# Kernel tuning notes

Hardware: AMD Instinct MI355X
Metric: run time of the kernel (lower is better)

The kernel has to match this reference:

```python
import jax, jax.numpy as jnp
import numpy as np

B, T = 2, 2048
V, C, H = 32000, 1024, 16
HS = C // H  # 64
W_SCALE = 0.02


def setup_inputs() -> dict:
    key = jax.random.key(0)
    ks = jax.random.split(key, 8)
    x = jax.random.randint(ks[0], (B, T), 0, V)
    tok_emb = jax.random.normal(ks[1], (V, C), jnp.float32) * W_SCALE
    pos_emb = jax.random.normal(ks[2], (T, C), jnp.float32) * W_SCALE
    wq = jax.random.normal(ks[3], (H, C, HS), jnp.float32) * W_SCALE
    wk = jax.random.normal(ks[4], (H, C, HS), jnp.float32) * W_SCALE
    wv = jax.random.normal(ks[5], (H, C, HS), jnp.float32) * W_SCALE
    bq = jnp.zeros((H, HS), jnp.float32)
    bk = jnp.zeros((H, HS), jnp.float32)
    bv = jnp.zeros((H, HS), jnp.float32)
    w_head = jax.random.normal(ks[6], (C, V), jnp.float32) * W_SCALE
    b_head = jnp.zeros((V,), jnp.float32)
    return dict(x=x, tok_emb=tok_emb, pos_emb=pos_emb, wq=wq, bq=bq,
                wk=wk, bk=bk, wv=wv, bv=bv, w_head=w_head, b_head=b_head)


def reference(x, tok_emb, pos_emb, wq, bq, wk, bk, wv, bv, w_head, b_head):
    Bx, Tx = x.shape
    Cx = tok_emb.shape[1]
    h = tok_emb[x] + pos_emb[:Tx]  # [B,T,C]
    # all heads batched: per-head Linear layers stacked on leading H axis
    q = jnp.einsum('btc,hcd->bhtd', h, wq) + bq[None, :, None, :]
    k = jnp.einsum('btc,hcd->bhtd', h, wk) + bk[None, :, None, :]
    v = jnp.einsum('btc,hcd->bhtd', h, wv) + bv[None, :, None, :]
    # NOTE: original scales by n_embd**-0.5 (full C), not head_size**-0.5
    att = jnp.einsum('bhtd,bhsd->bhts', q, k) * (Cx ** -0.5)
    causal = jnp.tril(jnp.ones((Tx, Tx), dtype=bool))
    att = jnp.where(causal, att, jnp.finfo(att.dtype).min)
    att = jax.nn.softmax(att, axis=-1)
    y = jnp.einsum('bhts,bhsd->bhtd', att, v)  # [B,H,T,HS]
    y = jnp.transpose(y, (0, 2, 1, 3)).reshape(Bx, Tx, Cx)  # concat heads
    logits = jnp.einsum('btc,cv->btv', y, w_head) + b_head  # [B,T,V]
    return logits
```

## Files before the change

kernel.cpp:

```cpp
#include <hip/hip_runtime.h>

#define T_SEQ 2048
#define C_DIM 1024
#define H_N   16
#define HS_D  64
#define V_DIM 32000

typedef float f32x4 __attribute__((ext_vector_type(4)));
typedef __bf16 bf16x8 __attribute__((ext_vector_type(8)));
typedef unsigned short us4 __attribute__((ext_vector_type(4)));
typedef unsigned short us8 __attribute__((ext_vector_type(8)));

__device__ inline unsigned short f2bf(float f) {
  unsigned int u = __float_as_uint(f);
  u = (u + 0x7FFFu + ((u >> 16) & 1u)) >> 16;
  return (unsigned short)u;
}

__global__ __launch_bounds__(256) void embed_kernel(
    const int* __restrict__ x, const float* __restrict__ tok,
    const float* __restrict__ pos, unsigned short* __restrict__ h) {
  int idx = blockIdx.x * 256 + threadIdx.x;
  int bt = idx >> 8;
  int c4 = (idx & 255) * 4;
  int t = bt & (T_SEQ - 1);
  int tokid = x[bt];
  f32x4 a = *(const f32x4*)(tok + (size_t)tokid * C_DIM + c4);
  f32x4 b = *(const f32x4*)(pos + (size_t)t * C_DIM + c4);
  f32x4 s = a + b;
  us4 o;
  o[0] = f2bf(s[0]); o[1] = f2bf(s[1]); o[2] = f2bf(s[2]); o[3] = f2bf(s[3]);
  *(us4*)(h + (size_t)bt * C_DIM + c4) = o;
}

__global__ __launch_bounds__(256) void repack_qkv(
    const float* __restrict__ wq, const float* __restrict__ wk, const float* __restrict__ wv,
    const float* __restrict__ bq, const float* __restrict__ bk, const float* __restrict__ bv,
    unsigned short* __restrict__ wt, float* __restrict__ biasp) {
  int which = blockIdx.y;
  const float* w = (which == 0) ? wq : (which == 1) ? wk : wv;
  int i = blockIdx.x * 256 + threadIdx.x;
  int d = i & 63;
  int c = (i >> 6) & (C_DIM - 1);
  int hh = i >> 16;
  int n = which * 1024 + hh * 64 + d;
  wt[(size_t)n * C_DIM + c] = f2bf(w[i]);
  if (c == 0) {
    const float* bb = (which == 0) ? bq : (which == 1) ? bk : bv;
    biasp[n] = bb[hh * 64 + d];
  }
}

__global__ __launch_bounds__(256) void repack_whead(
    const float* __restrict__ wh, unsigned short* __restrict__ wht) {
  __shared__ float tile[64][65];
  int v0 = blockIdx.x * 64;
  int c0 = blockIdx.y * 64;
  int tr = threadIdx.x >> 6;
  int tc = threadIdx.x & 63;
#pragma unroll
  for (int i = 0; i < 16; ++i) {
    int r = i * 4 + tr;
    tile[r][tc] = wh[(size_t)(c0 + r) * V_DIM + v0 + tc];
  }
  __syncthreads();
#pragma unroll
  for (int i = 0; i < 16; ++i) {
    int vr = i * 4 + tr;
    wht[(size_t)(v0 + vr) * C_DIM + c0 + tc] = f2bf(tile[tc][vr]);
  }
}

__global__ __launch_bounds__(256) void gemm_bf16(
    const unsigned short* __restrict__ A, const unsigned short* __restrict__ Bt,
    const float* __restrict__ bias, float* __restrict__ Cout, int N) {
  const int K = 1024;
  __shared__ unsigned short As[128 * 32];
  __shared__ unsigned short Bs[128 * 32];
  int tid = threadIdx.x;
  int lane = tid & 63, wvi = tid >> 6;
  int m0 = blockIdx.y * 128, n0 = blockIdx.x * 128;
  int wmm = (wvi >> 1) * 64, wnn = (wvi & 1) * 64;
  int r16 = lane & 15, gg = lane >> 4;
  f32x4 acc[4][4] = {};

  for (int k0 = 0; k0 < K; k0 += 32) {
#pragma unroll
    for (int it = 0; it < 2; ++it) {
      int ch = it * 256 + wvi * 64 + lane;
      int row = ch >> 2, cc = (ch & 3) * 8;
      const unsigned short* ga = A + (size_t)(m0 + row) * K + k0 + cc;
      __builtin_amdgcn_global_load_lds(
          (const __attribute__((address_space(1))) void*)ga,
          (__attribute__((address_space(3))) void*)&As[ch * 8], 16, 0, 0);
      const unsigned short* gb = Bt + (size_t)(n0 + row) * K + k0 + cc;
      __builtin_amdgcn_global_load_lds(
          (const __attribute__((address_space(1))) void*)gb,
          (__attribute__((address_space(3))) void*)&Bs[ch * 8], 16, 0, 0);
    }
    __syncthreads();
    bf16x8 fa[4], fb[4];
#pragma unroll
    for (int m = 0; m < 4; ++m)
      fa[m] = *(const bf16x8*)&As[(wmm + m * 16 + r16) * 32 + gg * 8];
#pragma unroll
    for (int n = 0; n < 4; ++n)
      fb[n] = *(const bf16x8*)&Bs[(wnn + n * 16 + r16) * 32 + gg * 8];
#pragma unroll
    for (int m = 0; m < 4; ++m)
#pragma unroll
      for (int n = 0; n < 4; ++n)
        acc[m][n] = __builtin_amdgcn_mfma_f32_16x16x32_bf16(fa[m], fb[n], acc[m][n], 0, 0, 0);
    __syncthreads();
  }
#pragma unroll
  for (int m = 0; m < 4; ++m) {
    int row = m0 + wmm + m * 16 + gg * 4;
#pragma unroll
    for (int n = 0; n < 4; ++n) {
      int col = n0 + wnn + n * 16 + r16;
      float bval = bias[col];
#pragma unroll
      for (int j = 0; j < 4; ++j)
        Cout[(size_t)(row + j) * N + col] = acc[m][n][j] + bval;
    }
  }
}

#define GK 1024
#define GNT 16

__global__ __launch_bounds__(512, 1) void gemm256(
    const unsigned short* __restrict__ A, const unsigned short* __restrict__ Bt,
    const float* __restrict__ bias, float* __restrict__ Cout, int N, int Mtiles) {
  __shared__ unsigned short As[2][256 * 64];
  __shared__ unsigned short Bs[2][256 * 64];
  int tid = threadIdx.x;
  int lane = tid & 63;
  int wid = tid >> 6;
  int wm = wid >> 2, wn = wid & 3;
  int l16 = lane & 15, g = lane >> 4;
  int swz = l16 & 7;

  int cpx = gridDim.x >> 3;
  int lin = blockIdx.x;
  int wg = (lin & 7) * cpx + (lin >> 3);
  int m0 = (wg % Mtiles) * 256;
  int n0 = (wg / Mtiles) * 256;

  auto stageA2 = [&](int kt, int mh) {
    unsigned short* lds = As[kt & 1];
#pragma unroll
    for (int q = 0; q < 2; ++q) {
      int chunk = q * 512 + tid;
      int rr = chunk >> 3;
      int row = (rr & 63) + ((rr >> 6) << 7) + mh * 64;
      int cpos = chunk & 7;
      int c = cpos ^ (row & 7);
      const unsigned short* src = A + (size_t)(m0 + row) * GK + kt * 64 + c * 8;
      __builtin_amdgcn_global_load_lds(
          (const __attribute__((address_space(1))) void*)src,
          (__attribute__((address_space(3))) void*)(lds + row * 64 + cpos * 8), 16, 0, 0);
    }
  };
  auto stageB4 = [&](int kt) {
    unsigned short* lds = Bs[kt & 1];
#pragma unroll
    for (int q = 0; q < 4; ++q) {
      int chunk = q * 512 + tid;
      int row = chunk >> 3;
      int cpos = chunk & 7;
      int c = cpos ^ (row & 7);
      const unsigned short* src = Bt + (size_t)(n0 + row) * GK + kt * 64 + c * 8;
      __builtin_amdgcn_global_load_lds(
          (const __attribute__((address_space(1))) void*)src,
          (__attribute__((address_space(3))) void*)(lds + row * 64 + cpos * 8), 16, 0, 0);
    }
  };

  stageA2(0, 0); stageB4(0);
  stageA2(0, 1);
  stageA2(1, 0); stageB4(1);
  asm volatile("s_waitcnt vmcnt(8)" ::: "memory");
  asm volatile("s_barrier" ::: "memory");

  f32x4 acc[8][4] = {};

  for (int t = 0; t < GNT; ++t) {
    const char* Ab = (const char*)As[t & 1];
    const char* Bb = (const char*)Bs[t & 1];
    bf16x8 bA[4][2], bB[4][2];

#pragma unroll
    for (int mi = 0; mi < 4; ++mi) {
      int row = wm * 128 + mi * 16 + l16;
#pragma unroll
      for (int kk = 0; kk < 2; ++kk)
        bA[mi][kk] = *(const bf16x8*)(Ab + row * 128 + (((kk * 4 + g) ^ swz) * 16));
    }
#pragma unroll
    for (int ni = 0; ni < 4; ++ni) {
      int row = wn * 64 + ni * 16 + l16;
#pragma unroll
      for (int kk = 0; kk < 2; ++kk)
        bB[ni][kk] = *(const bf16x8*)(Bb + row * 128 + (((kk * 4 + g) ^ swz) * 16));
    }
    if (t + 1 < GNT) stageA2(t + 1, 1);
    asm volatile("s_barrier" ::: "memory");
    asm volatile("s_waitcnt lgkmcnt(0)" ::: "memory");
    __builtin_amdgcn_sched_barrier(0);
    __builtin_amdgcn_s_setprio(1);
#pragma unroll
    for (int mi = 0; mi < 4; ++mi)
#pragma unroll
      for (int ni = 0; ni < 4; ++ni)
#pragma unroll
        for (int kk = 0; kk < 2; ++kk)
          acc[mi][ni] = __builtin_amdgcn_mfma_f32_16x16x32_bf16(bA[mi][kk], bB[ni][kk], acc[mi][ni], 0, 0, 0);
    __builtin_amdgcn_s_setprio(0);
    if (t + 1 < GNT) asm volatile("s_waitcnt vmcnt(8)" ::: "memory");
    else             asm volatile("s_waitcnt vmcnt(0)" ::: "memory");
    asm volatile("s_barrier" ::: "memory");

#pragma unroll
    for (int mi = 0; mi < 4; ++mi) {
      int row = wm * 128 + 64 + mi * 16 + l16;
#pragma unroll
      for (int kk = 0; kk < 2; ++kk)
        bA[mi][kk] = *(const bf16x8*)(Ab + row * 128 + (((kk * 4 + g) ^ swz) * 16));
    }
    if (t + 2 < GNT) { stageA2(t + 2, 0); stageB4(t + 2); }
    asm volatile("s_barrier" ::: "memory");
    asm volatile("s_waitcnt lgkmcnt(0)" ::: "memory");
    __builtin_amdgcn_sched_barrier(0);
    __builtin_amdgcn_s_setprio(1);
#pragma unroll
    for (int mi = 0; mi < 4; ++mi)
#pragma unroll
      for (int ni = 0; ni < 4; ++ni)
#pragma unroll
        for (int kk = 0; kk < 2; ++kk)
          acc[4 + mi][ni] = __builtin_amdgcn_mfma_f32_16x16x32_bf16(bA[mi][kk], bB[ni][kk], acc[4 + mi][ni], 0, 0, 0);
    __builtin_amdgcn_s_setprio(0);
    if (t + 2 < GNT)      asm volatile("s_waitcnt vmcnt(8)" ::: "memory");
    else if (t + 2 == GNT) asm volatile("s_waitcnt vmcnt(2)" ::: "memory");
    asm volatile("s_barrier" ::: "memory");
  }

#pragma unroll
  for (int mf = 0; mf < 8; ++mf) {
    int row = m0 + wm * 128 + mf * 16 + g * 4;
#pragma unroll
    for (int n = 0; n < 4; ++n) {
      int col = n0 + wn * 64 + n * 16 + l16;
      float bv = bias[col];
#pragma unroll
      for (int j = 0; j < 4; ++j)
        Cout[(size_t)(row + j) * N + col] = acc[mf][n][j] + bv;
    }
  }
}

__global__ __launch_bounds__(256) void attn_mfma(
    const float* __restrict__ qkv, unsigned short* __restrict__ y) {
  __shared__ char lds[24576];
  char* Kl = lds;
  char* Vl = lds + 8192;
  char* Pl = lds + 16384;

  int bh = blockIdx.y;
  int b = bh >> 4, h = bh & 15;
  int qb = (T_SEQ / 64 - 1) - blockIdx.x;
  int tid = threadIdx.x;
  int lane = tid & 63, w = tid >> 6;
  int l16 = lane & 15, g = lane >> 4;
  size_t bT = (size_t)b * T_SEQ;
  const float scale = 0.03125f;

  bf16x8 qf[2];
  {
    const float* qrow = qkv + (bT + qb * 64 + w * 16 + l16) * 3072 + h * 64;
#pragma unroll
    for (int kk = 0; kk < 2; ++kk) {
      f32x4 a = *(const f32x4*)(qrow + kk * 32 + g * 8);
      f32x4 c = *(const f32x4*)(qrow + kk * 32 + g * 8 + 4);
      us8 o;
      o[0] = f2bf(a[0]); o[1] = f2bf(a[1]); o[2] = f2bf(a[2]); o[3] = f2bf(a[3]);
      o[4] = f2bf(c[0]); o[5] = f2bf(c[1]); o[6] = f2bf(c[2]); o[7] = f2bf(c[3]);
      qf[kk] = *(bf16x8*)&o;
    }
  }

  f32x4 yacc[4] = {};
  float mrun[4], lrun[4];
#pragma unroll
  for (int j = 0; j < 4; ++j) { mrun[j] = -3.0e38f; lrun[j] = 0.f; }

  int srow = tid >> 2;
  int c0 = (tid & 3) * 16;

  for (int kb = 0; kb <= qb; ++kb) {
    {
      const float* kp = qkv + (bT + kb * 64 + srow) * 3072 + 1024 + h * 64 + c0;
      f32x4 k0 = *(const f32x4*)(kp + 0);
      f32x4 k1 = *(const f32x4*)(kp + 4);
      f32x4 k2 = *(const f32x4*)(kp + 8);
      f32x4 k3 = *(const f32x4*)(kp + 12);
      us8 pa, pb;
      pa[0]=f2bf(k0[0]); pa[1]=f2bf(k0[1]); pa[2]=f2bf(k0[2]); pa[3]=f2bf(k0[3]);
      pa[4]=f2bf(k1[0]); pa[5]=f2bf(k1[1]); pa[6]=f2bf(k1[2]); pa[7]=f2bf(k1[3]);
      pb[0]=f2bf(k2[0]); pb[1]=f2bf(k2[1]); pb[2]=f2bf(k2[2]); pb[3]=f2bf(k2[3]);
      pb[4]=f2bf(k3[0]); pb[5]=f2bf(k3[1]); pb[6]=f2bf(k3[2]); pb[7]=f2bf(k3[3]);
      *(us8*)(Kl + ((srow * 128 + c0 * 2)      ^ ((srow & 7) << 4))) = pa;
      *(us8*)(Kl + ((srow * 128 + c0 * 2 + 16) ^ ((srow & 7) << 4))) = pb;
      const float* vp = kp + 1024;
      f32x4 v0 = *(const f32x4*)(vp + 0);
      f32x4 v1 = *(const f32x4*)(vp + 4);
      f32x4 v2 = *(const f32x4*)(vp + 8);
      f32x4 v3 = *(const f32x4*)(vp + 12);
      float vals[16] = {v0[0],v0[1],v0[2],v0[3], v1[0],v1[1],v1[2],v1[3],
                        v2[0],v2[1],v2[2],v2[3], v3[0],v3[1],v3[2],v3[3]};
#pragma unroll
      for (int i = 0; i < 16; ++i) {
        int ch = c0 + i;
        *(unsigned short*)(Vl + ((ch * 128 + srow * 2) ^ ((ch & 7) << 4))) = f2bf(vals[i]);
      }
    }
    __syncthreads();

    f32x4 s[4] = {};
#pragma unroll
    for (int kk = 0; kk < 2; ++kk)
#pragma unroll
      for (int n = 0; n < 4; ++n) {
        int krow = n * 16 + l16;
        bf16x8 fb = *(const bf16x8*)(Kl + ((krow * 128 + (kk * 32 + g * 8) * 2) ^ ((krow & 7) << 4)));
        s[n] = __builtin_amdgcn_mfma_f32_16x16x32_bf16(qf[kk], fb, s[n], 0, 0, 0);
      }

    bool diag = (kb == qb);
    float pr[4][4];
    float corr[4];
#pragma unroll
    for (int j = 0; j < 4; ++j) {
      int rloc = w * 16 + g * 4 + j;
      float m = -3.0e38f;
#pragma unroll
      for (int n = 0; n < 4; ++n) {
        float v = s[n][j] * scale;
        if (diag && (n * 16 + l16) > rloc) v = -3.0e38f;
        pr[n][j] = v;
        m = fmaxf(m, v);
      }
      m = fmaxf(m, __shfl_xor(m, 1));
      m = fmaxf(m, __shfl_xor(m, 2));
      m = fmaxf(m, __shfl_xor(m, 4));
      m = fmaxf(m, __shfl_xor(m, 8));
      float mn = fmaxf(mrun[j], m);
      corr[j] = __expf(mrun[j] - mn);
      mrun[j] = mn;
      float ps = 0.f;
#pragma unroll
      for (int n = 0; n < 4; ++n) {
        float e = __expf(pr[n][j] - mn);
        pr[n][j] = e;
        ps += e;
      }
      ps += __shfl_xor(ps, 1);
      ps += __shfl_xor(ps, 2);
      ps += __shfl_xor(ps, 4);
      ps += __shfl_xor(ps, 8);
      lrun[j] = lrun[j] * corr[j] + ps;
    }
#pragma unroll
    for (int n = 0; n < 4; ++n)
#pragma unroll
      for (int j = 0; j < 4; ++j)
        yacc[n][j] *= corr[j];

#pragma unroll
    for (int j = 0; j < 4; ++j) {
      int row = w * 16 + g * 4 + j;
#pragma unroll
      for (int n = 0; n < 4; ++n)
        *(unsigned short*)(Pl + ((row * 128 + (n * 16 + l16) * 2) ^ ((row & 7) << 4))) = f2bf(pr[n][j]);
    }

#pragma unroll
    for (int kk = 0; kk < 2; ++kk) {
      int prow = w * 16 + l16;
      bf16x8 fa = *(const bf16x8*)(Pl + ((prow * 128 + (kk * 32 + g * 8) * 2) ^ ((prow & 7) << 4)));
#pragma unroll
      for (int n = 0; n < 4; ++n) {
        int vrow = n * 16 + l16;
        bf16x8 fb = *(const bf16x8*)(Vl + ((vrow * 128 + (kk * 32 + g * 8) * 2) ^ ((vrow & 7) << 4)));
        yacc[n] = __builtin_amdgcn_mfma_f32_16x16x32_bf16(fa, fb, yacc[n], 0, 0, 0);
      }
    }
    __syncthreads();
  }

#pragma unroll
  for (int j = 0; j < 4; ++j) {
    float inv = 1.0f / lrun[j];
    int row = qb * 64 + w * 16 + g * 4 + j;
    unsigned short* yo = y + (bT + row) * C_DIM + h * 64;
#pragma unroll
    for (int n = 0; n < 4; ++n)
      yo[n * 16 + l16] = f2bf(yacc[n][j] * inv);
  }
}

extern "C" void kernel_launch(void* const* d_in, const int* in_sizes, int n_in,
                              void* d_out, int out_size, void* d_ws, size_t ws_size,
                              hipStream_t stream) {
  const int*   x    = (const int*)d_in[0];
  const float* tok  = (const float*)d_in[1];
  const float* pos  = (const float*)d_in[2];
  const float* wq   = (const float*)d_in[3];
  const float* bq   = (const float*)d_in[4];
  const float* wk   = (const float*)d_in[5];
  const float* bk   = (const float*)d_in[6];
  const float* wv   = (const float*)d_in[7];
  const float* bv   = (const float*)d_in[8];
  const float* wh   = (const float*)d_in[9];
  const float* bhd  = (const float*)d_in[10];
  float* out = (float*)d_out;

  char* ws = (char*)d_ws;
  size_t off = 0;
  auto alloc = [&](size_t bytes) {
    void* p = ws + off;
    off += (bytes + 255) & ~(size_t)255;
    return p;
  };
  unsigned short* h_bf    = (unsigned short*)alloc((size_t)4096 * 1024 * 2);
  unsigned short* wqkv_t  = (unsigned short*)alloc((size_t)3072 * 1024 * 2);
  float*          qbias   = (float*)alloc((size_t)3072 * 4);
  unsigned short* wh_t    = (unsigned short*)alloc((size_t)V_DIM * 1024 * 2);
  float*          qkv     = (float*)alloc((size_t)4096 * 3072 * 4);
  unsigned short* ybf     = (unsigned short*)alloc((size_t)4096 * 1024 * 2);

  embed_kernel<<<4096, 256, 0, stream>>>(x, tok, pos, h_bf);
  repack_qkv<<<dim3(4096, 3), 256, 0, stream>>>(wq, wk, wv, bq, bk, bv, wqkv_t, qbias);
  repack_whead<<<dim3(V_DIM / 64, 16), 256, 0, stream>>>(wh, wh_t);
  gemm_bf16<<<dim3(3072 / 128, 4096 / 128), 256, 0, stream>>>(h_bf, wqkv_t, qbias, qkv, 3072);
  attn_mfma<<<dim3(T_SEQ / 64, 2 * H_N), 256, 0, stream>>>(qkv, ybf);
  gemm256<<<2000, 512, 0, stream>>>(ybf, wh_t, bhd, out, V_DIM, 16);
}
```

Measured before the change: 649.6 us.

## Emit bf16 QKV, pre-transpose V, and double-buffer K/V loads in attention

The QKV GEMM now writes bf16 instead of fp32, which halves its output traffic and removes the per-iteration fp32-to-bf16 conversion in attention. A new kernel transposes V per head into a contiguous layout so that attention can stage K and V directly into LDS with asynchronous global-to-LDS loads. Those loads are double-buffered, prefetching the next block while the current one is computed, and explicit waitcnt/barrier handle synchronisation. The cost is an extra kernel launch, an extra V buffer in memory, and more LDS per block.

```diff
diff --git a/kernel.cpp b/kernel.cpp
--- a/kernel.cpp
+++ b/kernel.cpp
@@ -71,9 +71,9 @@
   }
 }
 
-__global__ __launch_bounds__(256) void gemm_bf16(
+__global__ __launch_bounds__(256) void gemm_bf16_o16(
     const unsigned short* __restrict__ A, const unsigned short* __restrict__ Bt,
-    const float* __restrict__ bias, float* __restrict__ Cout, int N) {
+    const float* __restrict__ bias, unsigned short* __restrict__ Cout, int N) {
   const int K = 1024;
   __shared__ unsigned short As[128 * 32];
   __shared__ unsigned short Bs[128 * 32];
@@ -122,9 +122,29 @@
       float bval = bias[col];
 #pragma unroll
       for (int j = 0; j < 4; ++j)
-        Cout[(size_t)(row + j) * N + col] = acc[m][n][j] + bval;
-    }
-  }
+        Cout[(size_t)(row + j) * N + col] = f2bf(acc[m][n][j] + bval);
+    }
+  }
+}
+
+__global__ __launch_bounds__(256) void transpose_v(
+    const unsigned short* __restrict__ qkv, unsigned short* __restrict__ vt) {
+  __shared__ unsigned short tile[64][72];
+  int bh = blockIdx.y;
+  int b = bh >> 4, h = bh & 15;
+  int tb = blockIdx.x;
+  int r = threadIdx.x >> 2;
+  int c0 = (threadIdx.x & 3) * 16;
+  const unsigned short* src = qkv + ((size_t)(b * T_SEQ) + tb * 64 + r) * 3072 + 2048 + h * 64 + c0;
+  *(us8*)&tile[r][c0] = *(const us8*)src;
+  *(us8*)&tile[r][c0 + 8] = *(const us8*)(src + 8);
+  __syncthreads();
+  unsigned short* dst = vt + (size_t)bh * 64 * T_SEQ + (size_t)r * T_SEQ + tb * 64 + c0;
+  us8 o1, o2;
+#pragma unroll
+  for (int i = 0; i < 8; ++i) { o1[i] = tile[c0 + i][r]; o2[i] = tile[c0 + 8 + i][r]; }
+  *(us8*)dst = o1;
+  *(us8*)(dst + 8) = o2;
 }
 
 #define GK 1024
@@ -242,7 +262,7 @@
         for (int kk = 0; kk < 2; ++kk)
           acc[4 + mi][ni] = __builtin_amdgcn_mfma_f32_16x16x32_bf16(bA[mi][kk], bB[ni][kk], acc[4 + mi][ni], 0, 0, 0);
     __builtin_amdgcn_s_setprio(0);
-    if (t + 2 < GNT)      asm volatile("s_waitcnt vmcnt(8)" ::: "memory");
+    if (t + 2 < GNT)       asm volatile("s_waitcnt vmcnt(8)" ::: "memory");
     else if (t + 2 == GNT) asm volatile("s_waitcnt vmcnt(2)" ::: "memory");
     asm volatile("s_barrier" ::: "memory");
   }
@@ -262,11 +282,11 @@
 }
 
 __global__ __launch_bounds__(256) void attn_mfma(
-    const float* __restrict__ qkv, unsigned short* __restrict__ y) {
-  __shared__ char lds[24576];
-  char* Kl = lds;
-  char* Vl = lds + 8192;
-  char* Pl = lds + 16384;
+    const unsigned short* __restrict__ qkv, const unsigned short* __restrict__ vt,
+    unsigned short* __restrict__ y) {
+  __shared__ unsigned short Kl[2][4096];
+  __shared__ unsigned short Vl[2][4096];
+  __shared__ char Pl[8192];
 
   int bh = blockIdx.y;
   int b = bh >> 4, h = bh & 15;
@@ -277,56 +297,49 @@
   size_t bT = (size_t)b * T_SEQ;
   const float scale = 0.03125f;
 
-  bf16x8 qf[2];
-  {
-    const float* qrow = qkv + (bT + qb * 64 + w * 16 + l16) * 3072 + h * 64;
-#pragma unroll
-    for (int kk = 0; kk < 2; ++kk) {
-      f32x4 a = *(const f32x4*)(qrow + kk * 32 + g * 8);
-      f32x4 c = *(const f32x4*)(qrow + kk * 32 + g * 8 + 4);
-      us8 o;
-      o[0] = f2bf(a[0]); o[1] = f2bf(a[1]); o[2] = f2bf(a[2]); o[3] = f2bf(a[3]);
-      o[4] = f2bf(c[0]); o[5] = f2bf(c[1]); o[6] = f2bf(c[2]); o[7] = f2bf(c[3]);
-      qf[kk] = *(bf16x8*)&o;
-    }
-  }
+  const unsigned short* qrow = qkv + (bT + qb * 64 + w * 16 + l16) * 3072 + h * 64;
+  bf16x8 qf[2] = { *(const bf16x8*)(qrow + g * 8), *(const bf16x8*)(qrow + 32 + g * 8) };
 
   f32x4 yacc[4] = {};
   float mrun[4], lrun[4];
 #pragma unroll
   for (int j = 0; j < 4; ++j) { mrun[j] = -3.0e38f; lrun[j] = 0.f; }
 
-  int srow = tid >> 2;
-  int c0 = (tid & 3) * 16;
+  auto stageK = [&](int kb, int buf) {
+    const unsigned short* base = qkv + (bT + kb * 64) * 3072 + 1024 + h * 64;
+#pragma unroll
+    for (int q2 = 0; q2 < 2; ++q2) {
+      int chunk = q2 * 256 + tid;
+      int row = chunk >> 3, cpos = chunk & 7;
+      int c = cpos ^ (row & 7);
+      const unsigned short* src = base + (size_t)row * 3072 + c * 8;
+      __builtin_amdgcn_global_load_lds(
+          (const __attribute__((address_space(1))) void*)src,
+          (__attribute__((address_space(3))) void*)&Kl[buf][chunk * 8], 16, 0, 0);
+    }
+  };
+  auto stageV = [&](int kb, int buf) {
+    const unsigned short* base = vt + (size_t)bh * 64 * T_SEQ + kb * 64;
+#pragma unroll
+    for (int q2 = 0; q2 < 2; ++q2) {
+      int chunk = q2 * 256 + tid;
+      int row = chunk >> 3, cpos = chunk & 7;
+      int c = cpos ^ (row & 7);
+      const unsigned short* src = base + (size_t)row * T_SEQ + c * 8;
+      __builtin_amdgcn_global_load_lds(
+          (const __attribute__((address_space(1))) void*)src,
+          (__attribute__((address_space(3))) void*)&Vl[buf][chunk * 8], 16, 0, 0);
+    }
+  };
+
+  stageK(0, 0); stageV(0, 0);
 
   for (int kb = 0; kb <= qb; ++kb) {
-    {
-      const float* kp = qkv + (bT + kb * 64 + srow) * 3072 + 1024 + h * 64 + c0;
-      f32x4 k0 = *(const f32x4*)(kp + 0);
-      f32x4 k1 = *(const f32x4*)(kp + 4);
-      f32x4 k2 = *(const f32x4*)(kp + 8);
-      f32x4 k3 = *(const f32x4*)(kp + 12);
-      us8 pa, pb;
-      pa[0]=f2bf(k0[0]); pa[1]=f2bf(k0[1]); pa[2]=f2bf(k0[2]); pa[3]=f2bf(k0[3]);
-      pa[4]=f2bf(k1[0]); pa[5]=f2bf(k1[1]); pa[6]=f2bf(k1[2]); pa[7]=f2bf(k1[3]);
-      pb[0]=f2bf(k2[0]); pb[1]=f2bf(k2[1]); pb[2]=f2bf(k2[2]); pb[3]=f2bf(k2[3]);
-      pb[4]=f2bf(k3[0]); pb[5]=f2bf(k3[1]); pb[6]=f2bf(k3[2]); pb[7]=f2bf(k3[3]);
-      *(us8*)(Kl + ((srow * 128 + c0 * 2)      ^ ((srow & 7) << 4))) = pa;
-      *(us8*)(Kl + ((srow * 128 + c0 * 2 + 16) ^ ((srow & 7) << 4))) = pb;
-      const float* vp = kp + 1024;
-      f32x4 v0 = *(const f32x4*)(vp + 0);
-      f32x4 v1 = *(const f32x4*)(vp + 4);
-      f32x4 v2 = *(const f32x4*)(vp + 8);
-      f32x4 v3 = *(const f32x4*)(vp + 12);
-      float vals[16] = {v0[0],v0[1],v0[2],v0[3], v1[0],v1[1],v1[2],v1[3],
-                        v2[0],v2[1],v2[2],v2[3], v3[0],v3[1],v3[2],v3[3]};
-#pragma unroll
-      for (int i = 0; i < 16; ++i) {
-        int ch = c0 + i;
-        *(unsigned short*)(Vl + ((ch * 128 + srow * 2) ^ ((ch & 7) << 4))) = f2bf(vals[i]);
-      }
-    }
-    __syncthreads();
+    int buf = kb & 1;
+    if (kb < qb) { stageK(kb + 1, buf ^ 1); stageV(kb + 1, buf ^ 1); }
+    if (kb < qb) asm volatile("s_waitcnt vmcnt(4)" ::: "memory");
+    else         asm volatile("s_waitcnt vmcnt(0)" ::: "memory");
+    asm volatile("s_barrier" ::: "memory");
 
     f32x4 s[4] = {};
 #pragma unroll
@@ -334,7 +347,7 @@
 #pragma unroll
       for (int n = 0; n < 4; ++n) {
         int krow = n * 16 + l16;
-        bf16x8 fb = *(const bf16x8*)(Kl + ((krow * 128 + (kk * 32 + g * 8) * 2) ^ ((krow & 7) << 4)));
+        bf16x8 fb = *(const bf16x8*)((const char*)Kl[buf] + krow * 128 + (((kk * 4 + g) ^ (krow & 7)) * 16));
         s[n] = __builtin_amdgcn_mfma_f32_16x16x32_bf16(qf[kk], fb, s[n], 0, 0, 0);
       }
 
@@ -393,11 +406,11 @@
 #pragma unroll
       for (int n = 0; n < 4; ++n) {
         int vrow = n * 16 + l16;
-        bf16x8 fb = *(const bf16x8*)(Vl + ((vrow * 128 + (kk * 32 + g * 8) * 2) ^ ((vrow & 7) << 4)));
-        yacc[n] = __builtin_amdgcn_mfma_f32_16x16x32_bf16(fa, fb, yacc[n], 0, 0, 0);
+        bf16x8 fbv = *(const bf16x8*)((const char*)Vl[buf] + vrow * 128 + (((kk * 4 + g) ^ (vrow & 7)) * 16));
+        yacc[n] = __builtin_amdgcn_mfma_f32_16x16x32_bf16(fa, fbv, yacc[n], 0, 0, 0);
       }
     }
-    __syncthreads();
+    asm volatile("s_barrier" ::: "memory");
   }
 
 #pragma unroll
@@ -438,13 +451,15 @@
   unsigned short* wqkv_t  = (unsigned short*)alloc((size_t)3072 * 1024 * 2);
   float*          qbias   = (float*)alloc((size_t)3072 * 4);
   unsigned short* wh_t    = (unsigned short*)alloc((size_t)V_DIM * 1024 * 2);
-  float*          qkv     = (float*)alloc((size_t)4096 * 3072 * 4);
+  unsigned short* qkv_bf  = (unsigned short*)alloc((size_t)4096 * 3072 * 2);
+  unsigned short* vtb     = (unsigned short*)alloc((size_t)32 * 64 * T_SEQ * 2);
   unsigned short* ybf     = (unsigned short*)alloc((size_t)4096 * 1024 * 2);
 
   embed_kernel<<<4096, 256, 0, stream>>>(x, tok, pos, h_bf);
   repack_qkv<<<dim3(4096, 3), 256, 0, stream>>>(wq, wk, wv, bq, bk, bv, wqkv_t, qbias);
   repack_whead<<<dim3(V_DIM / 64, 16), 256, 0, stream>>>(wh, wh_t);
-  gemm_bf16<<<dim3(3072 / 128, 4096 / 128), 256, 0, stream>>>(h_bf, wqkv_t, qbias, qkv, 3072);
-  attn_mfma<<<dim3(T_SEQ / 64, 2 * H_N), 256, 0, stream>>>(qkv, ybf);
+  gemm_bf16_o16<<<dim3(3072 / 128, 4096 / 128), 256, 0, stream>>>(h_bf, wqkv_t, qbias, qkv_bf, 3072);
+  transpose_v<<<dim3(T_SEQ / 64, 2 * H_N), 256, 0, stream>>>(qkv_bf, vtb);
+  attn_mfma<<<dim3(T_SEQ / 64, 2 * H_N), 256, 0, stream>>>(qkv_bf, vtb, ybf);
   gemm256<<<2000, 512, 0, stream>>>(ybf, wh_t, bhd, out, V_DIM, 16);
 }
```

Measured after the change: 587.2 us. -9.6%, faster.
